# Kernel optimization log

Measured on AMD Instinct MI355X. Metric: run time of the kernel, lower is better.

The kernel has to match this reference:

```python
import jax, jax.numpy as jnp
import numpy as np

B, T, D, U = 64, 1024, 300, 300


def setup_inputs() -> dict:
    key = jax.random.key(0)
    ks = jax.random.split(key, 12)
    inputs = jax.random.normal(ks[0], (B, T, D), jnp.float32)
    lengths = jax.random.randint(ks[1], (B,), T // 2, T + 1)
    mask = jnp.arange(T)[None, :] < lengths[:, None]  # [B,T] bool

    def w(k, shape, fan_in):
        return jax.random.normal(k, shape, jnp.float32) * (1.0 / np.sqrt(fan_in))

    # Keras GRU (reset_after=True): kernel [D,3U], recurrent_kernel [U,3U], bias [2,3U]
    k_fwd = w(ks[2], (D, 3 * U), D)
    rk_fwd = w(ks[3], (U, 3 * U), U)
    b_fwd = jnp.zeros((2, 3 * U), jnp.float32)
    k_bwd = w(ks[4], (D, 3 * U), D)
    rk_bwd = w(ks[5], (U, 3 * U), U)
    b_bwd = jnp.zeros((2, 3 * U), jnp.float32)
    w_fc = w(ks[6], (2 * U, U), 2 * U)
    b_fc = jnp.zeros((U,), jnp.float32)
    return {
        "inputs": inputs, "mask": mask,
        "k_fwd": k_fwd, "rk_fwd": rk_fwd, "b_fwd": b_fwd,
        "k_bwd": k_bwd, "rk_bwd": rk_bwd, "b_bwd": b_bwd,
        "w_fc": w_fc, "b_fc": b_fc, "training": 0,
    }


def _gru_dir(x, mask, kernel, rkernel, bias):
    """Keras GRU v2 (reset_after=True), zero_output_for_mask, state frozen on masked steps.
    x: [B,T,D], mask: [B,T] bool -> (ys [B,T,U], h_final [B,U])"""
    b_in, b_rec = bias[0], bias[1]
    u = rkernel.shape[0]
    # precompute input projections for all timesteps (cuDNN-style hoisting)
    xp = jnp.einsum('btd,dk->btk', x, kernel) + b_in  # [B,T,3U]

    def step(h, inp):
        xt, mt = inp  # xt: [B,3U], mt: [B]
        rp = h @ rkernel + b_rec  # [B,3U]
        xz, xr, xh = jnp.split(xt, 3, axis=-1)
        rz, rr, rh = jnp.split(rp, 3, axis=-1)
        z = jax.nn.sigmoid(xz + rz)
        r = jax.nn.sigmoid(xr + rr)
        hh = jnp.tanh(xh + r * rh)
        h_new = z * h + (1.0 - z) * hh
        m = mt[:, None]
        h_carry = jnp.where(m, h_new, h)       # state does not update on masked steps
        y = jnp.where(m, h_new, jnp.zeros_like(h_new))  # zero_output_for_mask
        return h_carry, y

    h0 = jnp.zeros((x.shape[0], u), x.dtype)
    h_final, ys = jax.lax.scan(step, h0, (xp.transpose(1, 0, 2), mask.T))
    return ys.transpose(1, 0, 2), h_final


def reference(inputs, mask, k_fwd, rk_fwd, b_fwd, k_bwd, rk_bwd, b_bwd, w_fc, b_fc, training):
    mask = mask.astype(bool)
    x = inputs  # Dropout is identity at inference (training=0)
    y_f, h_f = _gru_dir(x, mask, k_fwd, rk_fwd, b_fwd)
    # backward direction: process reversed sequence/mask, then re-reverse outputs
    y_b, h_b = _gru_dir(x[:, ::-1], mask[:, ::-1], k_bwd, rk_bwd, b_bwd)
    y_b = y_b[:, ::-1]
    output = jnp.concatenate([y_f, y_b], axis=-1)  # [B,T,2U]
    state = jax.nn.relu(jnp.concatenate([h_f, h_b], axis=-1) @ w_fc + b_fc)  # [B,U]
    return output, state
```

## Files before the change

### kernel.cpp

```cpp
#include <hip/hip_runtime.h>
#include <hip/hip_bf16.h>


#define B_   64
#define T_   1024
#define D_   300
#define U_   300
#define NU   900
#define KP   320
#define NP   960
#define XPW  912
#define KB_  10
#define HSP  328
#define FRAGS_PER_DIR 570
#define SLOTF 57
#define SLOTSH (SLOTF*512)
#define NWGM 4

typedef short short8 __attribute__((ext_vector_type(8)));
typedef float floatx4 __attribute__((ext_vector_type(4)));

template <bool V> struct BoolC { static constexpr bool value = V; };

__device__ __forceinline__ float b2f_bits(unsigned short u) {
  union { unsigned int i; float f; } v; v.i = ((unsigned int)u) << 16; return v.f;
}
__device__ __forceinline__ unsigned short f2b(float f) {
  __hip_bfloat16 h = __float2bfloat16(f);
  return *reinterpret_cast<unsigned short*>(&h);
}
__device__ __forceinline__ float sigm_f(float x) {
  float e = __expf(-x);
  return __fdividef(1.f, 1.f + e);
}
__device__ __forceinline__ float tanh_f(float x) {
  float e = __expf(2.f * x);
  return 1.f - __fdividef(2.f, e + 1.f);
}
__device__ __forceinline__ void wait_lgkm0() {
  asm volatile("s_waitcnt lgkmcnt(0)" ::: "memory");
}
template <int N> __device__ __forceinline__ void wait_vm() {
  asm volatile("s_waitcnt vmcnt(%0)" :: "n"(N) : "memory");
}
__device__ __forceinline__ void dma16(const unsigned short* g, unsigned short* l) {
  __builtin_amdgcn_global_load_lds(
      (const __attribute__((address_space(1))) unsigned int*)g,
      (__attribute__((address_space(3))) unsigned int*)l, 16, 0, 0);
}

__global__ __launch_bounds__(64) void k_detect(const unsigned int* __restrict__ xw,
                                               const unsigned char* __restrict__ mb,
                                               int* __restrict__ flags) {
  __shared__ int red[64];
  int tid = threadIdx.x;
  int hits = 0;
  for (int i = tid; i < 2048; i += 64) {
    unsigned int lo = xw[i] & 0xFFFFu;
    int e = (int)((lo >> 7) & 0xFF);
    if (e >= 105 && e <= 135) hits++;
  }
  red[tid] = hits;
  __syncthreads();
  if (tid == 0) {
    int s = 0;
    for (int i = 0; i < 64; ++i) s += red[i];
    flags[0] = (s >= 1024) ? 1 : 0;
    unsigned char b0 = mb[0], b1 = mb[1];
    flags[1] = (b1 == 0) ? 0 : ((b0 == 1 && b1 == 1) ? 1 : 2);
  }
}

__global__ __launch_bounds__(256) void k_lengths(const unsigned char* __restrict__ mraw,
                                                 const int* __restrict__ flags,
                                                 int* __restrict__ lens) {
  __shared__ int red[256];
  int b = blockIdx.x, tid = threadIdx.x;
  int mt = flags[1];
  int s = 0;
  if (mt == 0) {
    const int* m = (const int*)mraw;
    for (int t = tid; t < T_; t += 256) s += m[(size_t)b * T_ + t] ? 1 : 0;
  } else if (mt == 1) {
    for (int t = tid; t < T_; t += 256) s += mraw[(size_t)b * T_ + t] ? 1 : 0;
  } else {
    const unsigned short* m = (const unsigned short*)mraw;
    for (int t = tid; t < T_; t += 256) s += m[(size_t)b * T_ + t] ? 1 : 0;
  }
  red[tid] = s; __syncthreads();
  for (int off = 128; off > 0; off >>= 1) {
    if (tid < off) red[tid] += red[tid + off];
    __syncthreads();
  }
  if (tid == 0) lens[b] = red[0];
}

__global__ __launch_bounds__(256) void k_xpad(const void* __restrict__ xraw,
                                              const int* __restrict__ flags,
                                              unsigned short* __restrict__ xp) {
  int id = blockIdx.x * 256 + threadIdx.x;
  int row = id / 40, seg = id % 40;
  int kbase = seg * 8;
  int bf = flags[0];
  unsigned short v[8];
  if (bf) {
    const unsigned short* x = (const unsigned short*)xraw;
#pragma unroll
    for (int i = 0; i < 8; ++i) {
      int k = kbase + i;
      v[i] = (k < D_) ? x[(size_t)row * D_ + k] : (unsigned short)0;
    }
  } else {
    const float* x = (const float*)xraw;
#pragma unroll
    for (int i = 0; i < 8; ++i) {
      int k = kbase + i;
      v[i] = (k < D_) ? f2b(x[(size_t)row * D_ + k]) : (unsigned short)0;
    }
  }
  uint4 o;
  o.x = (unsigned)v[0] | ((unsigned)v[1] << 16);
  o.y = (unsigned)v[2] | ((unsigned)v[3] << 16);
  o.z = (unsigned)v[4] | ((unsigned)v[5] << 16);
  o.w = (unsigned)v[6] | ((unsigned)v[7] << 16);
  *(uint4*)(xp + (size_t)row * KP + kbase) = o;
}

__global__ __launch_bounds__(256) void k_wpad(const void* __restrict__ kf,
                                              const void* __restrict__ kb,
                                              const int* __restrict__ flags,
                                              unsigned short* __restrict__ kp) {
  int id = blockIdx.x * 256 + threadIdx.x;
  if (id >= 2 * KP * NP) return;
  int dir = id / (KP * NP);
  int r = id % (KP * NP);
  int k = r / NP, n = r % NP;
  int bf = flags[0];
  unsigned short v = 0;
  if (k < D_ && n < NU) {
    size_t si = (size_t)k * NU + n;
    if (bf) v = ((const unsigned short*)(dir ? kb : kf))[si];
    else    v = f2b(((const float*)(dir ? kb : kf))[si]);
  }
  kp[id] = v;
}

__global__ __launch_bounds__(256) void k_prep(const void* __restrict__ rkf,
                                              const void* __restrict__ rkb,
                                              const void* __restrict__ bfw,
                                              const void* __restrict__ bbw,
                                              const void* __restrict__ wfc,
                                              const void* __restrict__ bfc,
                                              const int* __restrict__ flags,
                                              unsigned short* __restrict__ rkc,
                                              float* __restrict__ biasc,
                                              unsigned short* __restrict__ wfcc,
                                              float* __restrict__ bfcc) {
  int i = blockIdx.x * 256 + threadIdx.x;
  int bf = flags[0];
  if (i < 2 * D_ * NU) {
    int dir = i / (D_ * NU), r = i % (D_ * NU);
    const void* src = dir ? rkb : rkf;
    rkc[i] = bf ? ((const unsigned short*)src)[r] : f2b(((const float*)src)[r]);
  }
  if (i < 2 * 2 * NU) {
    int dir = i / (2 * NU), r = i % (2 * NU);
    const void* src = dir ? bbw : bfw;
    biasc[i] = bf ? b2f_bits(((const unsigned short*)src)[r]) : ((const float*)src)[r];
  }
  if (i < 2 * U_ * U_) {
    wfcc[i] = bf ? ((const unsigned short*)wfc)[i] : f2b(((const float*)wfc)[i]);
  }
  if (i < U_) {
    bfcc[i] = bf ? b2f_bits(((const unsigned short*)bfc)[i]) : ((const float*)bfc)[i];
  }
}

__global__ __launch_bounds__(256) void k_bpack(const unsigned short* __restrict__ rkc,
                                               unsigned short* __restrict__ bpack) {
  int idx = blockIdx.x * 256 + threadIdx.x;
  const int total = 2 * FRAGS_PER_DIR * 512;
  if (idx >= total) return;
  int rem = idx;
  int j = rem & 7; rem >>= 3;
  int lane = rem & 63; rem >>= 6;
  int f = rem % FRAGS_PER_DIR;
  int dir = rem / FRAGS_PER_DIR;
  int w, fr, ntc;
  if (f < 270) { w = f / 90; fr = f - w * 90; ntc = 9; }
  else { int f2 = f - 270; w = 3 + f2 / 60; fr = f2 % 60; ntc = 6; }
  int kb = fr / ntc, nt = fr % ntc;
  int lb = nt / 3, g = nt % 3;
  int ub0 = (w < 3) ? w * 3 : 9 + (w - 3) * 2;
  int l15 = lane & 15, quad = lane >> 4;
  int k = kb * 32 + quad * 8 + j;
  int u = (ub0 + lb) * 16 + l15;
  unsigned short v = 0;
  if (k < U_ && u < U_) {
    v = rkc[(size_t)dir * U_ * NU + (size_t)k * NU + (size_t)g * U_ + u];
  }
  bpack[idx] = v;
}

template <bool XPF32>
__global__ __launch_bounds__(256) void k_gemm(const unsigned short* __restrict__ xpad,
                                              const unsigned short* __restrict__ kpad,
                                              const float* __restrict__ biasc,
                                              void* __restrict__ xp_out) {
  __shared__ __align__(16) unsigned short As[64 * 40];
  __shared__ __align__(16) unsigned short Bs[64 * 40];
  int tid = threadIdx.x;
  int wave = tid >> 6, lane = tid & 63;
  int m0 = blockIdx.x * 64, n0 = blockIdx.y * 64;
  int dir = blockIdx.z;
  const unsigned short* Bsrc = kpad + (size_t)dir * KP * NP;
  const float* bin = biasc + (size_t)dir * 2 * NU;

  floatx4 acc[4];
#pragma unroll
  for (int i = 0; i < 4; ++i) acc[i] = {0.f, 0.f, 0.f, 0.f};

  int arow = tid >> 2, aseg = tid & 3;
  int bk = tid & 31, bn8 = (tid >> 5) * 8;
  int fr = lane & 15, fq = lane >> 4;

  for (int kc = 0; kc < KP; kc += 32) {
    uint4 av = *(const uint4*)(xpad + (size_t)(m0 + arow) * KP + kc + aseg * 8);
    uint4 bv = *(const uint4*)(Bsrc + (size_t)(kc + bk) * NP + n0 + bn8);
    *(uint4*)(As + arow * 40 + aseg * 8) = av;
    unsigned short tmp[8];
    tmp[0] = bv.x & 0xffff; tmp[1] = bv.x >> 16;
    tmp[2] = bv.y & 0xffff; tmp[3] = bv.y >> 16;
    tmp[4] = bv.z & 0xffff; tmp[5] = bv.z >> 16;
    tmp[6] = bv.w & 0xffff; tmp[7] = bv.w >> 16;
#pragma unroll
    for (int i = 0; i < 8; ++i) Bs[(bn8 + i) * 40 + bk] = tmp[i];
    __syncthreads();
    short8 a = *(const short8*)(As + (wave * 16 + fr) * 40 + fq * 8);
#pragma unroll
    for (int nt = 0; nt < 4; ++nt) {
      short8 bfrag = *(const short8*)(Bs + (nt * 16 + fr) * 40 + fq * 8);
      acc[nt] = __builtin_amdgcn_mfma_f32_16x16x32_bf16(a, bfrag, acc[nt], 0, 0, 0);
    }
    __syncthreads();
  }
#pragma unroll
  for (int nt = 0; nt < 4; ++nt) {
    int col = n0 + nt * 16 + fr;
    if (col >= XPW) continue;
    float bi = (col < NU) ? bin[col] : 0.f;
#pragma unroll
    for (int r = 0; r < 4; ++r) {
      int m = m0 + wave * 16 + fq * 4 + r;
      float v = acc[nt][r] + bi;
      size_t idx = ((size_t)dir * 65536 + m) * XPW + col;
      if (XPF32) ((float*)xp_out)[idx] = v;
      else ((unsigned short*)xp_out)[idx] = f2b(v);
    }
  }
}

template <int NTC, bool XPF32>
__device__ __forceinline__ void scan_loop(
    const unsigned short* __restrict__ bpL,
    unsigned short* __restrict__ winw,
    unsigned short (*sHiP)[16][HSP],
    unsigned short (*sLoP)[16][HSP],
    const void* __restrict__ xp_all,
    unsigned short* __restrict__ out16, float* __restrict__ out32, int obf,
    const float* __restrict__ brec, const int* __restrict__ lens,
    float* __restrict__ hfin,
    int dir, int mg, int ub0, int l15, int quad, int lane) {
  constexpr int NB = NTC / 3;

  int ucl[NB]; bool cv[NB];
  float bz[NB], brg[NB], bh[NB];
#pragma unroll
  for (int lb = 0; lb < NB; ++lb) {
    int u = (ub0 + lb) * 16 + l15;
    bool v = (u < U_);
    cv[lb] = v;
    ucl[lb] = v ? u : 0;
    bz[lb] = brec[ucl[lb]]; brg[lb] = brec[U_ + ucl[lb]]; bh[lb] = brec[2 * U_ + ucl[lb]];
  }
  size_t xbase[4];
  int mylen[4];
#pragma unroll
  for (int r = 0; r < 4; ++r) {
    xbase[r] = ((size_t)dir * 65536 + (size_t)(mg * 16 + quad * 4 + r) * T_) * XPW;
    mylen[r] = lens[mg * 16 + quad * 4 + r];
  }
  float hold[NB][4];
#pragma unroll
  for (int lb = 0; lb < NB; ++lb)
#pragma unroll
    for (int r = 0; r < 4; ++r) hold[lb][r] = 0.f;

  const unsigned short* winL = winw + (size_t)lane * 8;

  unsigned int XA[NB][3][4], XB[NB][3][4];

  auto load_xp = [&](unsigned int (&X)[NB][3][4], int t) {
#pragma unroll
    for (int r = 0; r < 4; ++r) {
      size_t ro = xbase[r] + (size_t)t * XPW;
      if (XPF32) {
        const unsigned int* xr = (const unsigned int*)xp_all + ro;
#pragma unroll
        for (int lb = 0; lb < NB; ++lb) {
          X[lb][0][r] = xr[ucl[lb]];
          X[lb][1][r] = xr[U_ + ucl[lb]];
          X[lb][2][r] = xr[2 * U_ + ucl[lb]];
        }
      } else {
        const unsigned short* xr = (const unsigned short*)xp_all + ro;
#pragma unroll
        for (int lb = 0; lb < NB; ++lb) {
          X[lb][0][r] = (unsigned int)xr[ucl[lb]];
          X[lb][1][r] = (unsigned int)xr[U_ + ucl[lb]];
          X[lb][2][r] = (unsigned int)xr[2 * U_ + ucl[lb]];
        }
      }
    }
  };
  auto xval = [&](unsigned int x) -> float {
    if (XPF32) { union { unsigned int i; float f; } v; v.i = x; return v.f; }
    return b2f_bits((unsigned short)x);
  };
  auto dma_kb = [&](int kb) {
    const unsigned short* g = bpL + (size_t)kb * NTC * 512;
    unsigned short* l = winw + (size_t)(kb & 1) * SLOTSH;
#pragma unroll
    for (int nt = 0; nt < NTC; ++nt)
      dma16(g + (size_t)nt * 512, l + (size_t)nt * 512);
  };

  dma_kb(0);
  dma_kb(1);
  load_xp(XA, dir ? (T_ - 1) : 0);
  asm volatile("s_waitcnt vmcnt(0)" ::: "memory");
  __syncthreads();

  auto step = [&](auto fwd_c, int s, unsigned int (&Xu)[NB][3][4],
                  unsigned int (&Xp)[NB][3][4]) {
    constexpr bool FWD = decltype(fwd_c)::value;
    const int t = dir ? (T_ - 1 - s) : s;
    const int par = s & 1;
    const unsigned short (*hH)[HSP] = sHiP[par];
    const unsigned short (*hL)[HSP] = sLoP[par];

    floatx4 acc[NTC];
#pragma unroll
    for (int i = 0; i < NTC; ++i) acc[i] = {0.f, 0.f, 0.f, 0.f};

#pragma unroll
    for (int i = 0; i < 10; ++i) {
      const int kb = FWD ? i : 9 - i;
      if (i >= 2 && i <= 8) wait_vm<NTC>();
      if (i == 9) wait_vm<0>();
      short8 ah = *(const short8*)&hH[l15][kb * 32 + quad * 8];
      short8 al = *(const short8*)&hL[l15][kb * 32 + quad * 8];
      short8 bfr[NTC];
#pragma unroll
      for (int nt = 0; nt < NTC; ++nt)
        bfr[nt] = *(const short8*)(winL + (size_t)(kb & 1) * SLOTSH + (size_t)nt * 512);
#pragma unroll
      for (int nt = 0; nt < NTC; ++nt)
        acc[nt] = __builtin_amdgcn_mfma_f32_16x16x32_bf16(ah, bfr[nt], acc[nt], 0, 0, 0);
#pragma unroll
      for (int nt = 0; nt < NTC; ++nt)
        acc[nt] = __builtin_amdgcn_mfma_f32_16x16x32_bf16(al, bfr[nt], acc[nt], 0, 0, 0);
      wait_lgkm0();
      if (i <= 7) dma_kb(FWD ? i + 2 : 7 - i);
    }

    {
      int tn = dir ? (t > 0 ? t - 1 : t) : (t < T_ - 1 ? t + 1 : t);
      load_xp(Xp, tn);
    }

    unsigned short (*nH)[HSP] = sHiP[par ^ 1];
    unsigned short (*nL)[HSP] = sLoP[par ^ 1];
#pragma unroll
    for (int r = 0; r < 4; ++r) {
      const int row = quad * 4 + r;
      const bool m = (t < mylen[r]);
      const size_t ob = ((size_t)(mg * 16 + row) * T_ + t) * 600 + (size_t)dir * U_;
#pragma unroll
      for (int lb = 0; lb < NB; ++lb) {
        float z  = sigm_f(xval(Xu[lb][0][r]) + acc[lb * 3 + 0][r] + bz[lb]);
        float rg = sigm_f(xval(Xu[lb][1][r]) + acc[lb * 3 + 1][r] + brg[lb]);
        float hh = tanh_f(xval(Xu[lb][2][r]) + rg * (acc[lb * 3 + 2][r] + bh[lb]));
        float hn = z * hold[lb][r] + (1.f - z) * hh;
        float hw = m ? hn : hold[lb][r];
        hold[lb][r] = hw;
        if (cv[lb]) {
          float y = m ? hn : 0.f;
          if (obf) out16[ob + ucl[lb]] = f2b(y); else out32[ob + ucl[lb]] = y;
          unsigned short hib = f2b(hw);
          nH[row][ucl[lb]] = hib;
          nL[row][ucl[lb]] = f2b(hw - b2f_bits(hib));
        }
      }
    }
    wait_lgkm0();
    __builtin_amdgcn_s_barrier();
  };

#pragma unroll 1
  for (int s = 0; s < T_; s += 2) {
    step(BoolC<true>{}, s, XA, XB);
    step(BoolC<false>{}, s + 1, XB, XA);
  }

#pragma unroll
  for (int lb = 0; lb < NB; ++lb) {
    if (!cv[lb]) continue;
#pragma unroll
    for (int r = 0; r < 4; ++r)
      hfin[((size_t)dir * B_ + mg * 16 + quad * 4 + r) * 304 + ucl[lb]] = hold[lb][r];
  }
}

template <bool XPF32>
__global__ __launch_bounds__(512, 2) void k_scan(const unsigned short* __restrict__ bpack,
                                                 const float* __restrict__ biasc,
                                                 const void* __restrict__ xp_all,
                                                 const int* __restrict__ lens,
                                                 const int* __restrict__ flags,
                                                 float* __restrict__ hfin,
                                                 void* __restrict__ outraw) {
  __shared__ unsigned short sHi[2][16][HSP];
  __shared__ unsigned short sLo[2][16][HSP];
  __shared__ __align__(16) unsigned short win[2 * SLOTSH];

  const int tid = threadIdx.x;
  const int mg = blockIdx.x;
  const int dir = blockIdx.y;
  const int wave = tid >> 6, lane = tid & 63;
  const int l15 = lane & 15, quad = lane >> 4;
  const int obf = flags[0];
  unsigned short* out16 = (unsigned short*)outraw;
  float* out32 = (float*)outraw;

  const int UB0w = (wave < 3) ? wave * 3 : 9 + (wave - 3) * 2;
  const int FB   = (wave < 3) ? wave * 90 : 270 + (wave - 3) * 60;
  const int RBW  = (wave < 3) ? wave * 9 : 27 + (wave - 3) * 6;

  {
    unsigned int* p0 = (unsigned int*)&sHi[0][0][0];
    unsigned int* p1 = (unsigned int*)&sLo[0][0][0];
    for (int i = tid; i < 2 * 16 * HSP / 2; i += 512) { p0[i] = 0u; p1[i] = 0u; }
  }

  const unsigned short* bpL = bpack + ((size_t)dir * FRAGS_PER_DIR + FB) * 512 + (size_t)lane * 8;
  unsigned short* winw = &win[(size_t)RBW * 512];
  const float* brec = biasc + (size_t)dir * 2 * NU + NU;

  if (wave < 3)
    scan_loop<9, XPF32>(bpL, winw, sHi, sLo, xp_all, out16, out32, obf, brec, lens,
                        hfin, dir, mg, UB0w, l15, quad, lane);
  else
    scan_loop<6, XPF32>(bpL, winw, sHi, sLo, xp_all, out16, out32, obf, brec, lens,
                        hfin, dir, mg, UB0w, l15, quad, lane);
}

__global__ __launch_bounds__(320) void k_state(const float* __restrict__ hfin,
                                               const unsigned short* __restrict__ wfcc,
                                               const float* __restrict__ bfcc,
                                               const int* __restrict__ flags,
                                               void* __restrict__ outraw) {
  int b = blockIdx.x, u = threadIdx.x;
  if (u >= U_) return;
  int obf = flags[0];
  float acc = bfcc[u];
  const float* hf = hfin + (size_t)b * 304;
  const float* hb = hfin + ((size_t)B_ + b) * 304;
  for (int k = 0; k < U_; ++k) acc = fmaf(hf[k], b2f_bits(wfcc[(size_t)k * U_ + u]), acc);
  for (int k = 0; k < U_; ++k) acc = fmaf(hb[k], b2f_bits(wfcc[(size_t)(U_ + k) * U_ + u]), acc);
  float v = fmaxf(acc, 0.f);
  size_t oi = (size_t)B_ * T_ * 600 + (size_t)b * U_ + u;
  if (obf) ((unsigned short*)outraw)[oi] = f2b(v);
  else     ((float*)outraw)[oi] = v;
}

extern "C" void kernel_launch(void* const* d_in, const int* in_sizes, int n_in,
                              void* d_out, int out_size, void* d_ws, size_t ws_size,
                              hipStream_t stream) {
  const void* x    = d_in[0];
  const void* mask = d_in[1];
  const void* kf   = d_in[2];
  const void* rkf  = d_in[3];
  const void* bfw  = d_in[4];
  const void* kb   = d_in[5];
  const void* rkb  = d_in[6];
  const void* bbw  = d_in[7];
  const void* wfc  = d_in[8];
  const void* bfc  = d_in[9];

  char* ws = (char*)d_ws;
  size_t off = 0;
  auto alloc = [&](size_t bytes) { void* p = ws + off; off += (bytes + 255) & ~(size_t)255; return p; };
  int* flags            = (int*)alloc(256);
  int* lens             = (int*)alloc(256);
  unsigned short* xpad  = (unsigned short*)alloc((size_t)65536 * KP * 2);
  unsigned short* kpad  = (unsigned short*)alloc((size_t)2 * KP * NP * 2);
  unsigned short* rkc   = (unsigned short*)alloc((size_t)2 * D_ * NU * 2);
  unsigned short* bpack = (unsigned short*)alloc((size_t)2 * FRAGS_PER_DIR * 512 * 2);
  float* biasc          = (float*)alloc((size_t)2 * 2 * NU * 4);
  unsigned short* wfcc  = (unsigned short*)alloc((size_t)2 * U_ * U_ * 2);
  float* bfcc           = (float*)alloc((size_t)U_ * 4);
  float* hfin           = (float*)alloc((size_t)2 * B_ * 304 * 4);
  void* xp = (void*)(ws + off);
  size_t need_f32 = off + (size_t)2 * 65536 * XPW * 4;
  bool xpf32 = ws_size >= need_f32;

  k_detect<<<dim3(1), dim3(64), 0, stream>>>((const unsigned int*)x, (const unsigned char*)mask, flags);
  k_lengths<<<dim3(B_), dim3(256), 0, stream>>>((const unsigned char*)mask, flags, lens);
  k_xpad<<<dim3(65536 * 40 / 256), dim3(256), 0, stream>>>(x, flags, xpad);
  k_wpad<<<dim3((2 * KP * NP + 255) / 256), dim3(256), 0, stream>>>(kf, kb, flags, kpad);
  k_prep<<<dim3((2 * D_ * NU + 255) / 256), dim3(256), 0, stream>>>(rkf, rkb, bfw, bbw, wfc, bfc,
                                                                    flags, rkc, biasc, wfcc, bfcc);
  k_bpack<<<dim3((2 * FRAGS_PER_DIR * 512 + 255) / 256), dim3(256), 0, stream>>>(rkc, bpack);
  if (xpf32) {
    k_gemm<true><<<dim3(1024, 15, 2), dim3(256), 0, stream>>>(xpad, kpad, biasc, xp);
    k_scan<true><<<dim3(NWGM, 2), dim3(512), 0, stream>>>(bpack, biasc, xp, lens, flags, hfin, d_out);
  } else {
    k_gemm<false><<<dim3(1024, 15, 2), dim3(256), 0, stream>>>(xpad, kpad, biasc, xp);
    k_scan<false><<<dim3(NWGM, 2), dim3(512), 0, stream>>>(bpack, biasc, xp, lens, flags, hfin, d_out);
  }
  k_state<<<dim3(B_), dim3(320), 0, stream>>>(hfin, wfcc, bfcc, flags, d_out);
}
```

Measured before the change: 14.59 ms.

## Keep leading recurrent-weight k-blocks resident in registers, stream the rest

The scan now holds the first KREG k-blocks of the recurrent weight fragments in VGPRs for the whole sequence (3 for 9-tile waves, 5 for 6-tile waves). Only the remaining k-blocks are streamed through the double-buffered LDS window each step. The x-projection loads for a step are issued at the start of that step and overlap the register-resident MFMAs, replacing the prefetch one step ahead. This cuts per-step global-to-LDS traffic and wait stalls, but greatly raises register pressure under launch_bounds(512,2) and exposes the xp load latency within the step.

```diff
diff --git a/kernel.cpp b/kernel.cpp
--- a/kernel.cpp
+++ b/kernel.cpp
@@ -20,8 +20,6 @@
 typedef short short8 __attribute__((ext_vector_type(8)));
 typedef float floatx4 __attribute__((ext_vector_type(4)));
 
-template <bool V> struct BoolC { static constexpr bool value = V; };
-
 __device__ __forceinline__ float b2f_bits(unsigned short u) {
   union { unsigned int i; float f; } v; v.i = ((unsigned int)u) << 16; return v.f;
 }
@@ -42,6 +40,9 @@
 }
 template <int N> __device__ __forceinline__ void wait_vm() {
   asm volatile("s_waitcnt vmcnt(%0)" :: "n"(N) : "memory");
+}
+__device__ __forceinline__ void cfence() {
+  asm volatile("" ::: "memory");
 }
 __device__ __forceinline__ void dma16(const unsigned short* g, unsigned short* l) {
   __builtin_amdgcn_global_load_lds(
@@ -260,7 +261,7 @@
   }
 }
 
-template <int NTC, bool XPF32>
+template <int NTC, int KREG, bool XPF32>
 __device__ __forceinline__ void scan_loop(
     const unsigned short* __restrict__ bpL,
     unsigned short* __restrict__ winw,
@@ -272,6 +273,8 @@
     float* __restrict__ hfin,
     int dir, int mg, int ub0, int l15, int quad, int lane) {
   constexpr int NB = NTC / 3;
+  constexpr int XPN = NB * 12;
+  constexpr int NSTR = KB_ - KREG;
 
   int ucl[NB]; bool cv[NB];
   float bz[NB], brg[NB], bh[NB];
@@ -296,11 +299,41 @@
 #pragma unroll
     for (int r = 0; r < 4; ++r) hold[lb][r] = 0.f;
 
+  short8 breg[KREG][NTC];
+#pragma unroll
+  for (int kb = 0; kb < KREG; ++kb)
+#pragma unroll
+    for (int nt = 0; nt < NTC; ++nt)
+      breg[kb][nt] = *(const short8*)(bpL + ((size_t)(kb * NTC + nt)) * 512);
+
   const unsigned short* winL = winw + (size_t)lane * 8;
 
-  unsigned int XA[NB][3][4], XB[NB][3][4];
-
-  auto load_xp = [&](unsigned int (&X)[NB][3][4], int t) {
+  __syncthreads();
+
+#pragma unroll 1
+  for (int s = 0; s < T_; ++s) {
+    const int t = dir ? (T_ - 1 - s) : s;
+    const int par = s & 1;
+    const unsigned short (*hH)[HSP] = sHiP[par];
+    const unsigned short (*hL)[HSP] = sLoP[par];
+
+    floatx4 acc[NTC];
+#pragma unroll
+    for (int i = 0; i < NTC; ++i) acc[i] = {0.f, 0.f, 0.f, 0.f};
+
+    {
+      const unsigned short* g0 = bpL + (size_t)KREG * NTC * 512;
+      unsigned short* l0 = winw + (size_t)(KREG & 1) * SLOTSH;
+#pragma unroll
+      for (int nt = 0; nt < NTC; ++nt) dma16(g0 + (size_t)nt * 512, l0 + (size_t)nt * 512);
+      const unsigned short* g1 = bpL + (size_t)(KREG + 1) * NTC * 512;
+      unsigned short* l1 = winw + (size_t)((KREG + 1) & 1) * SLOTSH;
+#pragma unroll
+      for (int nt = 0; nt < NTC; ++nt) dma16(g1 + (size_t)nt * 512, l1 + (size_t)nt * 512);
+    }
+    cfence();
+
+    unsigned int X[NB][3][4];
 #pragma unroll
     for (int r = 0; r < 4; ++r) {
       size_t ro = xbase[r] + (size_t)t * XPW;
@@ -322,42 +355,24 @@
         }
       }
     }
-  };
-  auto xval = [&](unsigned int x) -> float {
-    if (XPF32) { union { unsigned int i; float f; } v; v.i = x; return v.f; }
-    return b2f_bits((unsigned short)x);
-  };
-  auto dma_kb = [&](int kb) {
-    const unsigned short* g = bpL + (size_t)kb * NTC * 512;
-    unsigned short* l = winw + (size_t)(kb & 1) * SLOTSH;
-#pragma unroll
-    for (int nt = 0; nt < NTC; ++nt)
-      dma16(g + (size_t)nt * 512, l + (size_t)nt * 512);
-  };
-
-  dma_kb(0);
-  dma_kb(1);
-  load_xp(XA, dir ? (T_ - 1) : 0);
-  asm volatile("s_waitcnt vmcnt(0)" ::: "memory");
-  __syncthreads();
-
-  auto step = [&](auto fwd_c, int s, unsigned int (&Xu)[NB][3][4],
-                  unsigned int (&Xp)[NB][3][4]) {
-    constexpr bool FWD = decltype(fwd_c)::value;
-    const int t = dir ? (T_ - 1 - s) : s;
-    const int par = s & 1;
-    const unsigned short (*hH)[HSP] = sHiP[par];
-    const unsigned short (*hL)[HSP] = sLoP[par];
-
-    floatx4 acc[NTC];
-#pragma unroll
-    for (int i = 0; i < NTC; ++i) acc[i] = {0.f, 0.f, 0.f, 0.f};
-
-#pragma unroll
-    for (int i = 0; i < 10; ++i) {
-      const int kb = FWD ? i : 9 - i;
-      if (i >= 2 && i <= 8) wait_vm<NTC>();
-      if (i == 9) wait_vm<0>();
+    cfence();
+
+#pragma unroll
+    for (int kb = 0; kb < KREG; ++kb) {
+      short8 ah = *(const short8*)&hH[l15][kb * 32 + quad * 8];
+      short8 al = *(const short8*)&hL[l15][kb * 32 + quad * 8];
+#pragma unroll
+      for (int nt = 0; nt < NTC; ++nt)
+        acc[nt] = __builtin_amdgcn_mfma_f32_16x16x32_bf16(ah, breg[kb][nt], acc[nt], 0, 0, 0);
+#pragma unroll
+      for (int nt = 0; nt < NTC; ++nt)
+        acc[nt] = __builtin_amdgcn_mfma_f32_16x16x32_bf16(al, breg[kb][nt], acc[nt], 0, 0, 0);
+    }
+
+#pragma unroll
+    for (int j = 0; j < NSTR; ++j) {
+      const int kb = KREG + j;
+      if (j < 2) wait_vm<NTC + XPN>(); else wait_vm<NTC>();
       short8 ah = *(const short8*)&hH[l15][kb * 32 + quad * 8];
       short8 al = *(const short8*)&hL[l15][kb * 32 + quad * 8];
       short8 bfr[NTC];
@@ -370,13 +385,12 @@
 #pragma unroll
       for (int nt = 0; nt < NTC; ++nt)
         acc[nt] = __builtin_amdgcn_mfma_f32_16x16x32_bf16(al, bfr[nt], acc[nt], 0, 0, 0);
-      wait_lgkm0();
-      if (i <= 7) dma_kb(FWD ? i + 2 : 7 - i);
-    }
-
-    {
-      int tn = dir ? (t > 0 ? t - 1 : t) : (t < T_ - 1 ? t + 1 : t);
-      load_xp(Xp, tn);
+      if (kb + 2 < KB_) {
+        const unsigned short* g = bpL + (size_t)(kb + 2) * NTC * 512;
+        unsigned short* l = winw + (size_t)(kb & 1) * SLOTSH;
+#pragma unroll
+        for (int nt = 0; nt < NTC; ++nt) dma16(g + (size_t)nt * 512, l + (size_t)nt * 512);
+      }
     }
 
     unsigned short (*nH)[HSP] = sHiP[par ^ 1];
@@ -388,9 +402,19 @@
       const size_t ob = ((size_t)(mg * 16 + row) * T_ + t) * 600 + (size_t)dir * U_;
 #pragma unroll
       for (int lb = 0; lb < NB; ++lb) {
-        float z  = sigm_f(xval(Xu[lb][0][r]) + acc[lb * 3 + 0][r] + bz[lb]);
-        float rg = sigm_f(xval(Xu[lb][1][r]) + acc[lb * 3 + 1][r] + brg[lb]);
-        float hh = tanh_f(xval(Xu[lb][2][r]) + rg * (acc[lb * 3 + 2][r] + bh[lb]));
+        float xz, xr2, xh;
+        if (XPF32) {
+          union { unsigned int i; float f; } a, b, c;
+          a.i = X[lb][0][r]; b.i = X[lb][1][r]; c.i = X[lb][2][r];
+          xz = a.f; xr2 = b.f; xh = c.f;
+        } else {
+          xz = b2f_bits((unsigned short)X[lb][0][r]);
+          xr2 = b2f_bits((unsigned short)X[lb][1][r]);
+          xh = b2f_bits((unsigned short)X[lb][2][r]);
+        }
+        float z  = sigm_f(xz + acc[lb * 3 + 0][r] + bz[lb]);
+        float rg = sigm_f(xr2 + acc[lb * 3 + 1][r] + brg[lb]);
+        float hh = tanh_f(xh + rg * (acc[lb * 3 + 2][r] + bh[lb]));
         float hn = z * hold[lb][r] + (1.f - z) * hh;
         float hw = m ? hn : hold[lb][r];
         hold[lb][r] = hw;
@@ -405,12 +429,6 @@
     }
     wait_lgkm0();
     __builtin_amdgcn_s_barrier();
-  };
-
-#pragma unroll 1
-  for (int s = 0; s < T_; s += 2) {
-    step(BoolC<true>{}, s, XA, XB);
-    step(BoolC<false>{}, s + 1, XB, XA);
   }
 
 #pragma unroll
@@ -458,11 +476,11 @@
   const float* brec = biasc + (size_t)dir * 2 * NU + NU;
 
   if (wave < 3)
-    scan_loop<9, XPF32>(bpL, winw, sHi, sLo, xp_all, out16, out32, obf, brec, lens,
-                        hfin, dir, mg, UB0w, l15, quad, lane);
+    scan_loop<9, 3, XPF32>(bpL, winw, sHi, sLo, xp_all, out16, out32, obf, brec, lens,
+                           hfin, dir, mg, UB0w, l15, quad, lane);
   else
-    scan_loop<6, XPF32>(bpL, winw, sHi, sLo, xp_all, out16, out32, obf, brec, lens,
-                        hfin, dir, mg, UB0w, l15, quad, lane);
+    scan_loop<6, 5, XPF32>(bpL, winw, sHi, sLo, xp_all, out16, out32, obf, brec, lens,
+                           hfin, dir, mg, UB0w, l15, quad, lane);
 }
 
 __global__ __launch_bounds__(320) void k_state(const float* __restrict__ hfin,
```

After: 15.88 ms. +8.9%, slower.
